# Kernel tuning notes

Measured on AMD Instinct MI355X. Metric: run time of the kernel, lower is better.

The kernel has to match this reference:

```python
import jax, jax.numpy as jnp
import numpy as np

# RGA_Module(in_channel=128, in_spatial=784, use_spatial=True, use_channel=True,
#            cha_ratio=4, spa_ratio=4, down_ratio=4), BatchNorm in eval mode with
# running_mean=0, running_var=1 folded into per-channel scale/shift (s, b).
B, C, H, W = 64, 128, 28, 28
S = H * W            # 784
IC = C // 4          # 32  inter_channel
IS = S // 4          # 196 inter_spatial
DS = (1 + IS) // 4   # 49  W_spatial bottleneck
DC = (1 + IC) // 4   # 8   W_channel bottleneck


def setup_inputs() -> dict:
    key = jax.random.key(0)
    ks = iter(jax.random.split(key, 40))
    def wgt(shape):
        return jax.random.normal(next(ks), shape, jnp.float32) * 0.05
    def scale(c):
        return 1.0 + 0.1 * jax.random.normal(next(ks), (c,), jnp.float32)
    def shift(c):
        return 0.1 * jax.random.normal(next(ks), (c,), jnp.float32)

    inp = {"x": jax.random.normal(next(ks), (B, C, H, W), jnp.float32)}
    for name, shape in [("th_w", (IC, C)), ("ph_w", (IC, C)), ("ggs_w", (IS, 2 * S)),
                        ("gxs_w", (IC, C)), ("ws1_w", (DS, 1 + IS)), ("ws2_w", (1, DS)),
                        ("thc_w", (IS, S)), ("phc_w", (IS, S)), ("ggc_w", (IC, 2 * C)),
                        ("gxc_w", (IS, S)), ("wc1_w", (DC, 1 + IC)), ("wc2_w", (1, DC))]:
        inp[name] = wgt(shape)
    for name, ch in [("th", IC), ("ph", IC), ("ggs", IS), ("gxs", IC), ("ws1", DS),
                     ("ws2", 1), ("thc", IS), ("phc", IS), ("ggc", IC), ("gxc", IS),
                     ("wc1", DC), ("wc2", 1)]:
        inp[name + "_s"] = scale(ch)
        inp[name + "_b"] = shift(ch)
    return inp


def _bn(y, s, b):
    # eval-mode BatchNorm2d with running stats folded: per-channel affine
    return y * s[None, :, None, None] + b[None, :, None, None]


def _cbr(y, Wc, s, b):
    # 1x1 Conv (no bias) + BN(eval) + ReLU
    return jax.nn.relu(_bn(jnp.einsum('oc,bchw->bohw', Wc, y), s, b))


def reference(x, th_w, th_s, th_b, ph_w, ph_s, ph_b, ggs_w, ggs_s, ggs_b,
              gxs_w, gxs_s, gxs_b, ws1_w, ws1_s, ws1_b, ws2_w, ws2_s, ws2_b,
              thc_w, thc_s, thc_b, phc_w, phc_s, phc_b, ggc_w, ggc_s, ggc_b,
              gxc_w, gxc_s, gxc_b, wc1_w, wc1_s, wc1_b, wc2_w, wc2_s, wc2_b):
    b, c, h, w = x.shape
    hw = h * w
    # ---- spatial relation-aware attention ----
    theta = _cbr(x, th_w, th_s, th_b).reshape(b, -1, hw)   # [b, IC, hw]
    phi = _cbr(x, ph_w, ph_s, ph_b).reshape(b, -1, hw)     # [b, IC, hw]
    Gs = jnp.einsum('bci,bcj->bij', theta, phi)            # [b, hw, hw]
    Gs_in = jnp.transpose(Gs, (0, 2, 1)).reshape(b, hw, h, w)
    Gs_out = Gs.reshape(b, hw, h, w)
    Gs_joint = _cbr(jnp.concatenate([Gs_in, Gs_out], 1), ggs_w, ggs_s, ggs_b)  # [b, IS, h, w]
    g_xs = jnp.mean(_cbr(x, gxs_w, gxs_s, gxs_b), axis=1, keepdims=True)       # [b, 1, h, w]
    ys = jnp.concatenate([g_xs, Gs_joint], 1)                                  # [b, 1+IS, h, w]
    W_ys = _bn(jnp.einsum('oc,bchw->bohw', ws2_w, _cbr(ys, ws1_w, ws1_s, ws1_b)),
               ws2_s, ws2_b)                                                   # [b, 1, h, w]
    x = jax.nn.sigmoid(W_ys) * x
    # ---- channel relation-aware attention ----
    xc = jnp.transpose(x.reshape(b, c, hw), (0, 2, 1))[..., None]              # [b, hw, c, 1]
    theta_c = jnp.transpose(_cbr(xc, thc_w, thc_s, thc_b)[..., 0], (0, 2, 1))  # [b, c, IS]
    phi_c = _cbr(xc, phc_w, phc_s, phc_b)[..., 0]                              # [b, IS, c]
    Gc = jnp.einsum('bcs,bsd->bcd', theta_c, phi_c)                            # [b, c, c]
    Gc_joint = _cbr(jnp.concatenate([jnp.transpose(Gc, (0, 2, 1))[..., None],
                                     Gc[..., None]], 1), ggc_w, ggc_s, ggc_b)  # [b, IC, c, 1]
    g_xc = jnp.mean(_cbr(xc, gxc_w, gxc_s, gxc_b), axis=1, keepdims=True)      # [b, 1, c, 1]
    yc = jnp.concatenate([g_xc, Gc_joint], 1)                                  # [b, 1+IC, c, 1]
    W_yc = _bn(jnp.einsum('oc,bchw->bohw', wc2_w, _cbr(yc, wc1_w, wc1_s, wc1_b)),
               wc2_s, wc2_b)                                                   # [b, 1, c, 1]
    W_yc = jnp.transpose(W_yc, (0, 2, 1, 3))                                   # [b, c, 1, 1]
    return jax.nn.sigmoid(W_yc) * x
```

## Files before the change

### kernel.cpp

```cpp
#include <hip/hip_runtime.h>
#include <hip/hip_bf16.h>
#include <math.h>


#define BB 64
#define CC 128
#define HW 784
#define IC 32
#define IS 196
#define DS 49

#define O_THW 0
#define O_PHW 4096
#define O_GGSW 8192
#define O_GXSW 315520
#define O_WS1W 319616
#define O_WS2W 329272
#define O_THCW 329324
#define O_PHCW 482988
#define O_GGCW 636652
#define O_GXCW 644844
#define O_WC1W 798508
#define O_WC2W 798772
#define O_THS 798780
#define O_THB 798812
#define O_PHS 798844
#define O_PHB 798876
#define O_GGSS 798908
#define O_GGSB 799104
#define O_GXSS 799300
#define O_GXSB 799332
#define O_WS1S 799364
#define O_WS1B 799416
#define O_WS2S 799468
#define O_WS2B 799472
#define O_THCS 799476
#define O_THCB 799672
#define O_PHCS 799868
#define O_PHCB 800064
#define O_GGCS 800260
#define O_GGCB 800292
#define O_GXCS 800324
#define O_GXCB 800520
#define O_WC1S 800716
#define O_WC1B 800724
#define O_WC2S 800732
#define O_WC2B 800736
#define WF_TOTAL 800768

static const int SRC_SIZES[36] = {
  4096,4096,307328,4096,9653,49,153664,153664,8192,153664,264,8,
  32,32,32,32,196,196,32,32,49,49,1,1,196,196,196,196,32,32,196,196,8,8,1,1};
static const int DST_OFF[36] = {
  O_THW,O_PHW,O_GGSW,O_GXSW,O_WS1W,O_WS2W,O_THCW,O_PHCW,O_GGCW,O_GXCW,O_WC1W,O_WC2W,
  O_THS,O_THB,O_PHS,O_PHB,O_GGSS,O_GGSB,O_GXSS,O_GXSB,O_WS1S,O_WS1B,O_WS2S,O_WS2B,
  O_THCS,O_THCB,O_PHCS,O_PHCB,O_GGCS,O_GGCB,O_GXCS,O_GXCB,O_WC1S,O_WC1B,O_WC2S,O_WC2B};

struct ConvArgs { const void* p[36]; int cum[37]; int dst[36]; };

typedef __attribute__((ext_vector_type(8))) short short8;
typedef __attribute__((ext_vector_type(4))) float fragf4;

union FragU { unsigned int w[4]; short8 s8; };

__device__ __forceinline__ float sigf(float v){ return 1.0f/(1.0f+expf(-v)); }
__device__ __forceinline__ float hb2f(unsigned short h){ return __uint_as_float(((unsigned)h)<<16); }
__device__ __forceinline__ unsigned short f2hb(float v){
  __hip_bfloat16 hb = __float2bfloat16(v);
  return *reinterpret_cast<unsigned short*>(&hb);
}
__device__ __forceinline__ float loadx(const void* x, int flag, size_t idx){
  if (flag) return hb2f(((const unsigned short*)x)[idx]);
  return ((const float*)x)[idx];
}

__global__ void kd_detect(const void* x, int* flag){
  __shared__ int cnt[256];
  int t = threadIdx.x;
  const unsigned short* h = (const unsigned short*)x;
  int c = 0;
  for (int k=0;k<4;k++){
    unsigned short v = h[t*4+k];
    int e = (v>>7)&0xFF;
    c += (e==0 || (e>=97 && e<=157)) ? 1 : 0;
  }
  cnt[t] = c;
  __syncthreads();
  for (int s=128; s; s>>=1){ if (t<s) cnt[t]+=cnt[t+s]; __syncthreads(); }
  if (t==0) *flag = (cnt[0] >= 973) ? 1 : 0;
}

__global__ void kc_convert(ConvArgs a, const int* flagp, float* wf){
  int flag = *flagp;
  int g = blockIdx.x*256 + threadIdx.x;
  if (g >= a.cum[36]) return;
  int i = 0;
  while (g >= a.cum[i+1]) i++;
  int local = g - a.cum[i];
  float v;
  if (flag) v = hb2f(((const unsigned short*)a.p[i])[local]);
  else      v = ((const float*)a.p[i])[local];
  wf[a.dst[i] + local] = v;
}

#define KW_TOT (5*IS*HW + 96*CC)
#define KWK0_TOT (KW_TOT + 64*112)
__global__ void kw_wbf(const float* wf, unsigned short* wbf, unsigned int* ws1bf32){
  int i = blockIdx.x*256 + threadIdx.x;
  if (i >= KWK0_TOT) return;
  if (i < KW_TOT){
    float v;
    if (i < 3*IS*HW){
      int which = i/(IS*HW), r = i - which*(IS*HW);
      int off = which==0?O_THCW:(which==1?O_PHCW:O_GXCW);
      v = wf[off + r];
    } else if (i < 5*IS*HW){
      int which = i/(IS*HW), r = i - which*(IS*HW);
      int row = r/HW, col = r - row*HW;
      v = wf[O_GGSW + row*(2*HW) + (which-3)*HW + col];
    } else {
      int r = i - 5*IS*HW;
      int row = r >> 7, col = r & 127;
      v = (row < 64) ? wf[row*CC + col] : wf[O_GXSW + (row-64)*CC + col];
    }
    wbf[i] = f2hb(v);
  } else {
    int j = i - KW_TOT;
    int o2 = j/112, k2 = j - o2*112;
    int k = k2*2;
    float v0 = (o2<DS && k<197)   ? wf[O_WS1W + o2*197 + k]   : 0.f;
    float v1 = (o2<DS && k+1<197) ? wf[O_WS1W + o2*197 + k+1] : 0.f;
    ws1bf32[j] = (unsigned)f2hb(v0) | ((unsigned)f2hb(v1)<<16);
  }
}

#define XST 68
__global__ __launch_bounds__(256) void k1k2_mfma(const void* x, const int* flagp,
    const float* wf, const unsigned short* wthph, unsigned short* thph, float* g_xs)
{
  __shared__ __align__(16) unsigned int Xl[64*XST];
  int flag = *flagp;
  int t = threadIdx.x;
  int pt = blockIdx.x % 13, b = blockIdx.x / 13;
  int p0 = pt*64;

  #pragma unroll
  for (int k=0; k<8; k++){
    int idx = k*256 + t;
    int q = idx & 31;
    int c2 = idx >> 5;
    int p = p0 + 2*q, c = 2*c2;
    unsigned int w0 = 0u, w1 = 0u;
    if (p < HW){
      if (flag){
        const unsigned short* xb = (const unsigned short*)x + (size_t)b*CC*HW;
        unsigned int a0 = *(const unsigned int*)(xb + (size_t)c*HW + p);
        unsigned int a1 = *(const unsigned int*)(xb + (size_t)(c+1)*HW + p);
        w0 = (a0 & 0xffffu) | (a1 << 16);
        w1 = (a0 >> 16) | (a1 & 0xffff0000u);
      } else {
        const float* xb = (const float*)x + (size_t)b*CC*HW;
        float2 a0 = *(const float2*)(xb + (size_t)c*HW + p);
        float2 a1 = *(const float2*)(xb + (size_t)(c+1)*HW + p);
        w0 = (unsigned)f2hb(a0.x) | ((unsigned)f2hb(a1.x)<<16);
        w1 = (unsigned)f2hb(a0.y) | ((unsigned)f2hb(a1.y)<<16);
      }
    }
    Xl[(2*q+0)*XST + c2] = w0;
    Xl[(2*q+1)*XST + c2] = w1;
  }
  __syncthreads();

  int lane = t & 63, w = t >> 6;
  int m16 = lane & 15, kq = lane >> 4;
  fragf4 acc[6];
  #pragma unroll
  for (int mt=0; mt<6; mt++)
    #pragma unroll
    for (int r=0;r<4;r++) acc[mt][r] = 0.f;

  const unsigned short* Xu = (const unsigned short*)Xl;
  #pragma unroll
  for (int kk=0; kk<4; kk++){
    short8 bfr = *(const short8*)(Xu + (w*16+m16)*(2*XST) + kk*32 + kq*8);
    #pragma unroll
    for (int mt=0; mt<6; mt++){
      short8 af = *(const short8*)(wthph + (mt*16+m16)*CC + kk*32 + kq*8);
      acc[mt] = __builtin_amdgcn_mfma_f32_16x16x32_bf16(af, bfr, acc[mt], 0,0,0);
    }
  }

  int p = p0 + w*16 + m16;
  #pragma unroll
  for (int mt=0; mt<4; mt++){
    #pragma unroll
    for (int r=0;r<4;r++){
      int o = mt*16 + kq*4 + r;
      float sc = (o<32) ? wf[O_THS+o] : wf[O_PHS+o-32];
      float sh = (o<32) ? wf[O_THB+o] : wf[O_PHB+o-32];
      float v = fmaxf(sc*acc[mt][r] + sh, 0.f);
      if (p < HW) thph[((size_t)b*64 + o)*HW + p] = f2hb(v);
    }
  }
  float gs = 0.f;
  #pragma unroll
  for (int mt=4; mt<6; mt++){
    #pragma unroll
    for (int r=0;r<4;r++){
      int o = (mt-4)*16 + kq*4 + r;
      gs += fmaxf(wf[O_GXSS+o]*acc[mt][r] + wf[O_GXSB+o], 0.f);
    }
  }
  gs += __shfl_xor(gs, 16);
  gs += __shfl_xor(gs, 32);
  if (kq == 0 && p < HW) g_xs[(size_t)b*HW + p] = gs*(1.f/32.f);
}

#define K3ST 40
__global__ __launch_bounds__(256) void k3_mfma(const unsigned short* wggs,
    const unsigned short* thph, unsigned short* acomb)
{
  __shared__ __align__(16) unsigned short Al[112*K3ST];
  __shared__ __align__(16) unsigned short Bl[32*K3ST];
  int t = threadIdx.x;
  int mh = blockIdx.x & 1;
  int b  = (blockIdx.x >> 1) & 63;
  int which = blockIdx.x >> 7;
  int m0 = mh*112;
  const unsigned short* wsrc = wggs + (size_t)which*IS*HW;
  const unsigned short* ssrc = thph + ((size_t)b*64 + (which ? 0 : 32))*HW;
  int lane = t & 63, w = t >> 6;
  int m16 = lane & 15, kq = lane >> 4;
  fragf4 acc[2][2];
  #pragma unroll
  for (int i=0;i<2;i++)
    #pragma unroll
    for (int nt=0;nt<2;nt++)
      #pragma unroll
      for (int r=0;r<4;r++) acc[i][nt][r] = 0.f;

  for (int kk=0; kk<25; kk++){
    int p0 = kk*32;
    __syncthreads();
    for (int i=t; i<112*4; i+=256){
      int row = i>>2, q = i&3;
      uint4 v = make_uint4(0u,0u,0u,0u);
      int gr = m0 + row, p = p0 + q*8;
      if (gr < IS && p+8 <= HW)
        v = *(const uint4*)(wsrc + (size_t)gr*HW + p);
      *(uint4*)(Al + row*K3ST + q*8) = v;
    }
    if (t < 128){
      int row = t>>2, q = t&3;
      uint4 v = make_uint4(0u,0u,0u,0u);
      int p = p0 + q*8;
      if (p+8 <= HW)
        v = *(const uint4*)(ssrc + (size_t)row*HW + p);
      *(uint4*)(Bl + row*K3ST + q*8) = v;
    }
    __syncthreads();
    short8 bfr[2];
    #pragma unroll
    for (int nt=0;nt<2;nt++)
      bfr[nt] = *(const short8*)(Bl + (nt*16+m16)*K3ST + kq*8);
    #pragma unroll
    for (int i=0;i<2;i++){
      int mt = w + 4*i;
      if (mt < 7){
        short8 af = *(const short8*)(Al + (mt*16+m16)*K3ST + kq*8);
        acc[i][0] = __builtin_amdgcn_mfma_f32_16x16x32_bf16(af, bfr[0], acc[i][0], 0,0,0);
        acc[i][1] = __builtin_amdgcn_mfma_f32_16x16x32_bf16(af, bfr[1], acc[i][1], 0,0,0);
      }
    }
  }
  unsigned short* dst = acomb + (size_t)b*208*64 + which*32;
  #pragma unroll
  for (int i=0;i<2;i++){
    int mt = w + 4*i;
    if (mt >= 7) continue;
    #pragma unroll
    for (int r=0;r<4;r++){
      int o = m0 + mt*16 + kq*4 + r;
      if (o >= 208) continue;
      #pragma unroll
      for (int nt=0;nt<2;nt++){
        int c = nt*16 + m16;
        dst[(size_t)o*64 + c] = (o < IS) ? f2hb(acc[i][nt][r]) : (unsigned short)0;
      }
    }
  }
}

#define A4ST 72
#define ALS 33
#define GTS 113
union K4Sh {
  struct { unsigned short Al16[208*A4ST]; unsigned int Sl[64*ALS]; } s1;
  unsigned int Gt[64*GTS];
};
__global__ __launch_bounds__(256,3) void k4_mfma(const void* x, const int* flagp,
    const float* wf, const unsigned short* thph,
    const unsigned short* acomb, const float* g_xs,
    const unsigned int* ws1bf32, unsigned short* x1tp)
{
  __shared__ K4Sh sh;
  __shared__ float ash[64];
  int flag = *flagp;
  int t = threadIdx.x;
  int pt = blockIdx.x % 13, b = blockIdx.x / 13;
  int p0 = pt*64;
  int lane = t & 63, w = t >> 6;
  int col = lane & 15, kq = lane >> 4;

  const unsigned short* Ab16 = acomb + (size_t)b*208*64;
  for (int i=t; i<208*8; i+=256){
    int row = i>>3, q = i&7;
    uint4 v = make_uint4(0u,0u,0u,0u);
    if (row < IS) v = *(const uint4*)(Ab16 + (size_t)row*64 + q*8);
    *(uint4*)(sh.s1.Al16 + (size_t)row*A4ST + q*8) = v;
  }
  const unsigned short* tb = thph + (size_t)b*64*HW;
  for (int i=t; i<32*32; i+=256){
    int c2 = i>>5, q = i&31;
    int p = p0 + 2*q;
    unsigned int w0 = 0u, w1 = 0u;
    if (p < HW){
      int c = 2*c2;
      unsigned int a0 = *(const unsigned int*)(tb + (size_t)c*HW + p);
      unsigned int a1 = *(const unsigned int*)(tb + (size_t)(c+1)*HW + p);
      w0 = (a0 & 0xffffu) | (a1 << 16);
      w1 = (a0 >> 16) | (a1 & 0xffff0000u);
    }
    sh.s1.Sl[(2*q+0)*ALS + c2] = w0;
    sh.s1.Sl[(2*q+1)*ALS + c2] = w1;
  }
  __syncthreads();

  fragf4 acc1[13];
  #pragma unroll
  for (int nt=0; nt<13; nt++)
    #pragma unroll
    for (int r=0;r<4;r++) acc1[nt][r] = 0.f;
  #pragma unroll
  for (int kk=0; kk<2; kk++){
    FragU af;
    #pragma unroll
    for (int q=0;q<4;q++) af.w[q] = sh.s1.Sl[(w*16+col)*ALS + kk*16 + kq*4 + q];
    #pragma unroll
    for (int nt=0; nt<13; nt++){
      short8 bf8 = *(const short8*)(sh.s1.Al16 + (size_t)(nt*16+col)*A4ST + kk*32 + kq*8);
      acc1[nt] = __builtin_amdgcn_mfma_f32_16x16x32_bf16(af.s8, bf8, acc1[nt], 0,0,0);
    }
  }
  __syncthreads();

  unsigned short* Gt16 = (unsigned short*)sh.Gt;
  for (int i=t; i<64*9; i+=256){
    int pp = i/9, q = i - pp*9;
    sh.Gt[pp*GTS + 104 + q] = 0u;
  }
  if (t < 64){
    int p = p0 + t;
    float gx = (p < HW) ? g_xs[b*HW + p] : 0.f;
    Gt16[t*226 + 0] = f2hb(gx);
  }
  #pragma unroll
  for (int nt=0; nt<13; nt++){
    int o = nt*16 + col;
    float sc = wf[O_GGSS + o], shf = wf[O_GGSB + o];
    #pragma unroll
    for (int r=0;r<4;r++){
      int pp = w*16 + kq*4 + r;
      float g = fmaxf(sc*acc1[nt][r] + shf, 0.f);
      Gt16[pp*226 + 1 + o] = f2hb(g);
    }
  }
  __syncthreads();

  fragf4 acc2[4];
  #pragma unroll
  for (int nt=0; nt<4; nt++)
    #pragma unroll
    for (int r=0;r<4;r++) acc2[nt][r] = 0.f;
  #pragma unroll
  for (int kk=0; kk<7; kk++){
    FragU af;
    #pragma unroll
    for (int q=0;q<4;q++) af.w[q] = sh.Gt[(w*16+col)*GTS + kk*16 + kq*4 + q];
    #pragma unroll
    for (int nt=0; nt<4; nt++){
      FragU bf;
      #pragma unroll
      for (int q=0;q<4;q++) bf.w[q] = ws1bf32[(nt*16+col)*112 + kk*16 + kq*4 + q];
      acc2[nt] = __builtin_amdgcn_mfma_f32_16x16x32_bf16(af.s8, bf.s8, acc2[nt], 0,0,0);
    }
  }

  float wys[4] = {0.f,0.f,0.f,0.f};
  #pragma unroll
  for (int nt=0; nt<4; nt++){
    int o2 = nt*16 + col;
    bool vd = (o2 < DS);
    float s1 = vd ? wf[O_WS1S+o2] : 0.f;
    float b1 = vd ? wf[O_WS1B+o2] : 0.f;
    float w2 = vd ? wf[O_WS2W+o2] : 0.f;
    #pragma unroll
    for (int r=0;r<4;r++){
      float z = fmaxf(s1*acc2[nt][r] + b1, 0.f);
      wys[r] += w2*z;
    }
  }
  #pragma unroll
  for (int m=1; m<16; m<<=1){
    #pragma unroll
    for (int r=0;r<4;r++) wys[r] += __shfl_xor(wys[r], m, 16);
  }
  if (col == 0){
    float s2 = wf[O_WS2S], b2 = wf[O_WS2B];
    #pragma unroll
    for (int r=0;r<4;r++){
      int pp = w*16 + kq*4 + r;
      ash[pp] = sigf(s2*wys[r] + b2);
    }
  }
  __syncthreads();

  for (int i=t; i<CC*16; i+=256){
    int c = i>>4, q = i&15;
    int p = p0 + q*4;
    if (p < HW){
      float a0 = ash[q*4+0], a1 = ash[q*4+1], a2 = ash[q*4+2], a3 = ash[q*4+3];
      size_t base = (size_t)b*CC*HW + (size_t)c*HW + p;
      float v0,v1,v2,v3;
      if (flag){
        uint2 u = *(const uint2*)((const unsigned short*)x + base);
        v0 = a0*hb2f((unsigned short)(u.x & 0xffff));
        v1 = a1*hb2f((unsigned short)(u.x >> 16));
        v2 = a2*hb2f((unsigned short)(u.y & 0xffff));
        v3 = a3*hb2f((unsigned short)(u.y >> 16));
      } else {
        float4 xv = *(const float4*)((const float*)x + base);
        v0 = a0*xv.x; v1 = a1*xv.y; v2 = a2*xv.z; v3 = a3*xv.w;
      }
      uint2 o2;
      o2.x = (unsigned)f2hb(v0) | ((unsigned)f2hb(v1)<<16);
      o2.y = (unsigned)f2hb(v2) | ((unsigned)f2hb(v3)<<16);
      *(uint2*)(x1tp + base) = o2;
    }
  }
}

#define KST 40
__global__ __launch_bounds__(256) void k8_mfma(const unsigned short* wbf,
    const unsigned short* x1tp, const float* wf, float* outp)
{
  __shared__ __align__(16) unsigned short Al[48*KST];
  __shared__ __align__(16) unsigned short Bl[128*KST];
  int t = threadIdx.x;
  int j = blockIdx.x & 63;
  int b = (j&7)*8 + (j>>3);
  int mt = blockIdx.x >> 6;
  int m0 = mt*48;
  const unsigned short* xsrc = x1tp + (size_t)b*CC*HW;
  int lane = t & 63, w = t >> 6;
  int m16 = lane & 15, kq = lane >> 4;
  fragf4 acc[3][2];
  #pragma unroll
  for (int st=0; st<3; st++)
    #pragma unroll
    for (int ct=0; ct<2; ct++)
      #pragma unroll
      for (int r=0; r<4; r++) acc[st][ct][r] = 0.f;

  for (int kk=0; kk<25; kk++){
    int p0 = kk*32;
    __syncthreads();
    if (t < 192){
      int row = t>>2, q = t&3;
      uint4 v = make_uint4(0u,0u,0u,0u);
      int g = m0 + row, p = p0 + q*8;
      if (g < 3*IS && p+8 <= HW)
        v = *(const uint4*)(wbf + (size_t)g*HW + p);
      *(uint4*)(Al + row*KST + q*8) = v;
    }
    for (int i=t; i<128*4; i+=256){
      int row = i>>2, q = i&3;
      uint4 v = make_uint4(0u,0u,0u,0u);
      int p = p0 + q*8;
      if (p+8 <= HW)
        v = *(const uint4*)(xsrc + (size_t)row*HW + p);
      *(uint4*)(Bl + row*KST + q*8) = v;
    }
    __syncthreads();
    short8 bfr[2];
    #pragma unroll
    for (int ct=0; ct<2; ct++){
      int n = (w*2+ct)*16 + m16;
      bfr[ct] = *(const short8*)(Bl + n*KST + kq*8);
    }
    #pragma unroll
    for (int st=0; st<3; st++){
      short8 af = *(const short8*)(Al + (st*16+m16)*KST + kq*8);
      acc[st][0] = __builtin_amdgcn_mfma_f32_16x16x32_bf16(af, bfr[0], acc[st][0], 0,0,0);
      acc[st][1] = __builtin_amdgcn_mfma_f32_16x16x32_bf16(af, bfr[1], acc[st][1], 0,0,0);
    }
  }
  #pragma unroll
  for (int st=0; st<3; st++){
    #pragma unroll
    for (int r=0; r<4; r++){
      int g = m0 + st*16 + kq*4 + r;
      if (g >= 3*IS) continue;
      int which = (g >= 2*IS) ? 2 : (g >= IS ? 1 : 0);
      int s = g - which*IS;
      int so = (which==2) ? O_GXCS : O_THCS + which*392;
      float sc = wf[so + s], sh = wf[so + 196 + s];
      float* dst = outp + (size_t)which*(64*IS*CC) + ((size_t)b*IS + s)*CC;
      #pragma unroll
      for (int ct=0; ct<2; ct++){
        int c = (w*2+ct)*16 + m16;
        dst[c] = fmaxf(sc*acc[st][ct][r] + sh, 0.f);
      }
    }
  }
}

__global__ __launch_bounds__(256) void k9_bfact(const float* wf, const float* thcp,
    const float* phcp, float* Bph, float* Bth)
{
  __shared__ __align__(16) float wtl[32*32*4];
  int t = threadIdx.x;
  int sq = blockIdx.x & 3;
  int b  = (blockIdx.x >> 2) & 63;
  int which = blockIdx.x >> 8;
  for (int i = t; i < 32*32; i += 256){
    int jc = i >> 5, o = i & 31;
    *(float4*)(wtl + i*4) =
        *(const float4*)(wf + O_GGCW + o*256 + which*CC + jc*4);
  }
  __syncthreads();
  const float* src = which ? thcp : phcp;
  float* dst = which ? Bth : Bph;
  int o = t & 31, sloc = t >> 5;
  int s0 = sq*49;
  float acc[7];
  #pragma unroll
  for (int k=0;k<7;k++) acc[k]=0.f;
  const float* srow[7];
  #pragma unroll
  for (int k=0;k<7;k++){
    int sl = sloc + 8*k;
    srow[k] = src + ((size_t)b*IS + s0 + (sl<49 ? sl : 0))*CC;
  }
  for (int jc=0; jc<32; jc++){
    float4 wv = *(const float4*)(wtl + (jc*32+o)*4);
    #pragma unroll
    for (int k=0;k<7;k++){
      if (sloc + 8*k < 49){
        float4 sv = *(const float4*)(srow[k] + jc*4);
        acc[k] += wv.x*sv.x + wv.y*sv.y + wv.z*sv.z + wv.w*sv.w;
      }
    }
  }
  #pragma unroll
  for (int k=0;k<7;k++){
    int sl = sloc + 8*k;
    if (sl < 49){
      dst[((size_t)b*IS + s0 + sl)*IC + o] = acc[k];
    }
  }
}

__global__ __launch_bounds__(256) void k10a_part(const float* thcp, const float* phcp,
    const float* gxcp, const float* Bph, const float* Bth,
    float* part, float* gxp)
{
  int t = threadIdx.x;
  int d = t & 127, oh = t >> 7;
  int sc = blockIdx.x % 14, b = blockIdx.x / 14;
  int s0 = sc*14;
  float acc[16];
  #pragma unroll
  for (int o=0;o<16;o++) acc[o]=0.f;
  float gxa = 0.f;
  for (int i=0;i<14;i++){
    int s = s0 + i;
    size_t base = ((size_t)b*IS + s)*CC + d;
    float tv = thcp[base], pv = phcp[base];
    if (oh == 0) gxa += gxcp[base];
    const float* bp = Bph + ((size_t)b*IS + s)*IC + oh*16;
    const float* bt = Bth + ((size_t)b*IS + s)*IC + oh*16;
    #pragma unroll
    for (int o=0;o<16;o++) acc[o] += bp[o]*tv + bt[o]*pv;
  }
  float* pb = part + (((size_t)b*14 + sc)*IC + oh*16)*CC + d;
  #pragma unroll
  for (int o=0;o<16;o++) pb[(size_t)o*CC] = acc[o];
  if (oh == 0) gxp[((size_t)b*14 + sc)*CC + d] = gxa;
}

__global__ void k10b_catt(const float* wf, const float* part, const float* gxp,
                          float* c_att)
{
  int idx = blockIdx.x*256 + threadIdx.x;
  int d = idx & 127;
  int b = idx >> 7;
  float acc[IC];
  #pragma unroll
  for (int o=0;o<IC;o++) acc[o]=0.f;
  float gx = 0.f;
  for (int sc=0; sc<14; sc++){
    gx += gxp[((size_t)b*14 + sc)*CC + d];
    const float* pb = part + ((size_t)b*14 + sc)*IC*CC + d;
    #pragma unroll
    for (int o=0;o<IC;o++) acc[o] += pb[(size_t)o*CC];
  }
  gx *= (1.f/196.f);
  #pragma unroll
  for (int o=0;o<IC;o++) acc[o] = fmaxf(wf[O_GGCS+o]*acc[o]+wf[O_GGCB+o], 0.f);
  float acc2 = 0.f;
  #pragma unroll
  for (int o2=0;o2<8;o2++){
    float tt = wf[O_WC1W + o2*33]*gx;
    #pragma unroll
    for (int o=0;o<IC;o++) tt += wf[O_WC1W + o2*33+1+o]*acc[o];
    float z = fmaxf(wf[O_WC1S+o2]*tt + wf[O_WC1B+o2], 0.f);
    acc2 += wf[O_WC2W+o2]*z;
  }
  c_att[idx] = sigf(wf[O_WC2S]*acc2 + wf[O_WC2B]);
}

__global__ void k12_final(const int* flagp, const uint4* x1tp4,
                          const float* c_att, void* out)
{
  int i = blockIdx.x*256 + threadIdx.x;
  int flag = *flagp;
  uint4 v = x1tp4[i];
  float a = c_att[i/98];
  float f[8];
  f[0] = a*hb2f((unsigned short)(v.x & 0xffff));
  f[1] = a*hb2f((unsigned short)(v.x >> 16));
  f[2] = a*hb2f((unsigned short)(v.y & 0xffff));
  f[3] = a*hb2f((unsigned short)(v.y >> 16));
  f[4] = a*hb2f((unsigned short)(v.z & 0xffff));
  f[5] = a*hb2f((unsigned short)(v.z >> 16));
  f[6] = a*hb2f((unsigned short)(v.w & 0xffff));
  f[7] = a*hb2f((unsigned short)(v.w >> 16));
  if (flag){
    uint4 o;
    o.x = (unsigned)f2hb(f[0]) | ((unsigned)f2hb(f[1])<<16);
    o.y = (unsigned)f2hb(f[2]) | ((unsigned)f2hb(f[3])<<16);
    o.z = (unsigned)f2hb(f[4]) | ((unsigned)f2hb(f[5])<<16);
    o.w = (unsigned)f2hb(f[6]) | ((unsigned)f2hb(f[7])<<16);
    ((uint4*)out)[i] = o;
  } else {
    float4* op = (float4*)out + (size_t)i*2;
    op[0] = make_float4(f[0], f[1], f[2], f[3]);
    op[1] = make_float4(f[4], f[5], f[6], f[7]);
  }
}

extern "C" void kernel_launch(void* const* d_in, const int* in_sizes, int n_in,
                              void* d_out, int out_size, void* d_ws, size_t ws_size,
                              hipStream_t stream)
{
  const void* x = d_in[0];

  float* W = (float*)d_ws;
  int*   flag  = (int*)W;
  float* wf    = W + 64;
  float* theta = wf + WF_TOTAL;
  unsigned short* thph = (unsigned short*)(theta + 1605632);
  float* g_xs  = theta + 2*1605632;
  float* Aphi  = g_xs + 50176;
  float* Atheta= Aphi + 401408;
  unsigned short* acomb = (unsigned short*)Aphi;
  unsigned short* x1tp = (unsigned short*)(Atheta + 401408);
  float* thcp  = Atheta + 401408 + 3211264;
  float* phcp  = thcp + 1605632;
  float* gxcp  = phcp + 1605632;
  float* Bph   = gxcp + 1605632;
  float* Bth   = Bph + 401408;
  unsigned int* ws1bf32 = (unsigned int*)(Bth + 401408);
  float* c_att = (float*)(ws1bf32) + 9664;
  unsigned short* wbf = (unsigned short*)(c_att + 8192);
  unsigned short* wggs = wbf + 3*IS*HW;
  unsigned short* wthph = wbf + 5*IS*HW;
  float* part = theta;
  float* gxp  = theta + 3670016;

  ConvArgs ca;
  ca.cum[0] = 0;
  for (int i=0;i<36;i++){
    ca.p[i] = d_in[i+1];
    ca.cum[i+1] = ca.cum[i] + SRC_SIZES[i];
    ca.dst[i] = DST_OFF[i];
  }

  kd_detect<<<1, 256, 0, stream>>>(x, flag);
  kc_convert<<<(800716+255)/256, 256, 0, stream>>>(ca, flag, wf);
  kw_wbf<<<(KWK0_TOT+255)/256, 256, 0, stream>>>(wf, wbf, ws1bf32);
  k1k2_mfma<<<64*13, 256, 0, stream>>>(x, flag, wf, wthph, thph, g_xs);
  k3_mfma<<<2*64*2, 256, 0, stream>>>(wggs, thph, acomb);
  k4_mfma<<<64*13, 256, 0, stream>>>(x, flag, wf, thph, acomb,
      g_xs, ws1bf32, x1tp);
  k8_mfma<<<13*64, 256, 0, stream>>>(wbf, x1tp, wf, thcp);
  k9_bfact<<<2*64*4, 256, 0, stream>>>(wf, thcp, phcp, Bph, Bth);
  k10a_part<<<64*14, 256, 0, stream>>>(thcp, phcp, gxcp, Bph, Bth, part, gxp);
  k10b_catt<<<(BB*CC)/256, 256, 0, stream>>>(wf, part, gxp, c_att);
  k12_final<<<(BB*CC*HW/8)/256, 256, 0, stream>>>(flag, (const uint4*)x1tp,
      c_att, d_out);
}
```

Baseline: 332.9 us.

## Double-buffer k8 GEMM tiles with register prefetch; prefetch x early in gate kernel

Measured after the change: 329.1 us. About the same (-1.2%).

```diff
diff --git a/kernel.cpp b/kernel.cpp
--- a/kernel.cpp
+++ b/kernel.cpp
@@ -334,6 +334,26 @@
     sh.s1.Sl[(2*q+0)*ALS + c2] = w0;
     sh.s1.Sl[(2*q+1)*ALS + c2] = w1;
   }
+  float4 xf[8]; uint2 xh[8];
+  if (flag){
+    #pragma unroll
+    for (int jj=0; jj<8; jj++){
+      int i = jj*256 + t;
+      int c = i>>4, q = i&15;
+      int p = p0 + q*4;
+      size_t base = (size_t)b*CC*HW + (size_t)c*HW + (p < HW ? p : 0);
+      xh[jj] = *(const uint2*)((const unsigned short*)x + base);
+    }
+  } else {
+    #pragma unroll
+    for (int jj=0; jj<8; jj++){
+      int i = jj*256 + t;
+      int c = i>>4, q = i&15;
+      int p = p0 + q*4;
+      size_t base = (size_t)b*CC*HW + (size_t)c*HW + (p < HW ? p : 0);
+      xf[jj] = *(const float4*)((const float*)x + base);
+    }
+  }
   __syncthreads();
 
   fragf4 acc1[13];
@@ -425,7 +445,9 @@
   }
   __syncthreads();
 
-  for (int i=t; i<CC*16; i+=256){
+  #pragma unroll
+  for (int jj=0; jj<8; jj++){
+    int i = jj*256 + t;
     int c = i>>4, q = i&15;
     int p = p0 + q*4;
     if (p < HW){
@@ -433,13 +455,13 @@
       size_t base = (size_t)b*CC*HW + (size_t)c*HW + p;
       float v0,v1,v2,v3;
       if (flag){
-        uint2 u = *(const uint2*)((const unsigned short*)x + base);
+        uint2 u = xh[jj];
         v0 = a0*hb2f((unsigned short)(u.x & 0xffff));
         v1 = a1*hb2f((unsigned short)(u.x >> 16));
         v2 = a2*hb2f((unsigned short)(u.y & 0xffff));
         v3 = a3*hb2f((unsigned short)(u.y >> 16));
       } else {
-        float4 xv = *(const float4*)((const float*)x + base);
+        float4 xv = xf[jj];
         v0 = a0*xv.x; v1 = a1*xv.y; v2 = a2*xv.z; v3 = a3*xv.w;
       }
       uint2 o2;
@@ -454,8 +476,8 @@
 __global__ __launch_bounds__(256) void k8_mfma(const unsigned short* wbf,
     const unsigned short* x1tp, const float* wf, float* outp)
 {
-  __shared__ __align__(16) unsigned short Al[48*KST];
-  __shared__ __align__(16) unsigned short Bl[128*KST];
+  __shared__ __align__(16) unsigned short Al[2][48*KST];
+  __shared__ __align__(16) unsigned short Bl[2][128*KST];
   int t = threadIdx.x;
   int j = blockIdx.x & 63;
   int b = (j&7)*8 + (j>>3);
@@ -464,6 +486,12 @@
   const unsigned short* xsrc = x1tp + (size_t)b*CC*HW;
   int lane = t & 63, w = t >> 6;
   int m16 = lane & 15, kq = lane >> 4;
+  int ar = t>>2, aq8 = (t&3)*8;
+  bool aok = (t < 192) && (m0 + ar < 3*IS);
+  const unsigned short* arow = wbf + (size_t)(m0 + ar)*HW + aq8;
+  const unsigned short* brow0 = xsrc + (size_t)ar*HW + aq8;
+  const unsigned short* brow1 = xsrc + (size_t)(ar+64)*HW + aq8;
+
   fragf4 acc[3][2];
   #pragma unroll
   for (int st=0; st<3; st++)
@@ -472,37 +500,49 @@
       #pragma unroll
       for (int r=0; r<4; r++) acc[st][ct][r] = 0.f;
 
+  uint4 va = make_uint4(0u,0u,0u,0u), vb0, vb1;
+  if (aok) va = *(const uint4*)(arow);
+  vb0 = *(const uint4*)(brow0);
+  vb1 = *(const uint4*)(brow1);
+  if (t < 192) *(uint4*)(&Al[0][ar*KST + aq8]) = va;
+  *(uint4*)(&Bl[0][ar*KST + aq8]) = vb0;
+  *(uint4*)(&Bl[0][(ar+64)*KST + aq8]) = vb1;
+  __syncthreads();
+  va = make_uint4(0u,0u,0u,0u);
+  if (aok) va = *(const uint4*)(arow + 32);
+  vb0 = *(const uint4*)(brow0 + 32);
+  vb1 = *(const uint4*)(brow1 + 32);
+
+  int cur = 0;
   for (int kk=0; kk<25; kk++){
-    int p0 = kk*32;
-    __syncthreads();
-    if (t < 192){
-      int row = t>>2, q = t&3;
-      uint4 v = make_uint4(0u,0u,0u,0u);
-      int g = m0 + row, p = p0 + q*8;
-      if (g < 3*IS && p+8 <= HW)
-        v = *(const uint4*)(wbf + (size_t)g*HW + p);
-      *(uint4*)(Al + row*KST + q*8) = v;
-    }
-    for (int i=t; i<128*4; i+=256){
-      int row = i>>2, q = i&3;
-      uint4 v = make_uint4(0u,0u,0u,0u);
-      int p = p0 + q*8;
-      if (p+8 <= HW)
-        v = *(const uint4*)(xsrc + (size_t)row*HW + p);
-      *(uint4*)(Bl + row*KST + q*8) = v;
-    }
-    __syncthreads();
     short8 bfr[2];
     #pragma unroll
-    for (int ct=0; ct<2; ct++){
-      int n = (w*2+ct)*16 + m16;
-      bfr[ct] = *(const short8*)(Bl + n*KST + kq*8);
-    }
+    for (int ct=0; ct<2; ct++)
+      bfr[ct] = *(const short8*)(&Bl[cur][((w*2+ct)*16+m16)*KST + kq*8]);
     #pragma unroll
     for (int st=0; st<3; st++){
-      short8 af = *(const short8*)(Al + (st*16+m16)*KST + kq*8);
+      short8 af = *(const short8*)(&Al[cur][(st*16+m16)*KST + kq*8]);
       acc[st][0] = __builtin_amdgcn_mfma_f32_16x16x32_bf16(af, bfr[0], acc[st][0], 0,0,0);
       acc[st][1] = __builtin_amdgcn_mfma_f32_16x16x32_bf16(af, bfr[1], acc[st][1], 0,0,0);
+    }
+    if (kk < 24){
+      if (t < 192) *(uint4*)(&Al[cur^1][ar*KST + aq8]) = va;
+      *(uint4*)(&Bl[cur^1][ar*KST + aq8]) = vb0;
+      *(uint4*)(&Bl[cur^1][(ar+64)*KST + aq8]) = vb1;
+      __syncthreads();
+      if (kk < 23){
+        int off = (kk+2)*32;
+        bool pok = (kk < 22) || ((t&3) < 2);
+        va = make_uint4(0u,0u,0u,0u);
+        vb0 = make_uint4(0u,0u,0u,0u);
+        vb1 = make_uint4(0u,0u,0u,0u);
+        if (pok){
+          if (aok) va = *(const uint4*)(arow + off);
+          vb0 = *(const uint4*)(brow0 + off);
+          vb1 = *(const uint4*)(brow1 + off);
+        }
+      }
+      cur ^= 1;
     }
   }
   #pragma unroll
```
